# Optimization experiments

Hardware: AMD Instinct MI355X
Metric: run time of the kernel (lower is better)

## Reference

```python
import jax, jax.numpy as jnp
import numpy as np

# Static config matching init_kwargs / input_specs
B, CIN, H, W = 4, 64, 128, 128
COUT, K, DG = 64, 3, 8
STRIDE, PAD, DIL = 1, 1, 1
HO = (H + 2 * PAD - DIL * (K - 1) - 1) // STRIDE + 1
WO = (W + 2 * PAD - DIL * (K - 1) - 1) // STRIDE + 1
KK = K * K
CG = CIN // DG  # channels per deformable group


def setup_inputs() -> dict:
    key = jax.random.key(0)
    k1, k2, k3, k4 = jax.random.split(key, 4)
    x = jax.random.normal(k1, (B, CIN, H, W), jnp.float32)
    offset = jax.random.normal(k2, (B, 2 * DG * KK, HO, WO), jnp.float32)
    s = 1.0 / np.sqrt(CIN * KK)  # matches reset_parameters stdv / fan_in bound
    weight = jax.random.uniform(k3, (COUT, CIN, K, K), jnp.float32, -s, s)
    bias = jax.random.uniform(k4, (COUT,), jnp.float32, -s, s)
    return {"x": x, "offset": offset, "weight": weight, "bias": bias}


def _deform_conv(x, offset, weight, bias):
    # offset layout (DCNv1): [B, DG * KK * 2, Ho, Wo], per kernel point (dy, dx)
    off = offset.reshape(B, DG, KK, 2, HO, WO)
    khs = (jnp.repeat(jnp.arange(K), K) * DIL).astype(jnp.float32)  # [KK] kernel dy
    kws = (jnp.tile(jnp.arange(K), K) * DIL).astype(jnp.float32)    # [KK] kernel dx
    gy = (jnp.arange(HO) * STRIDE - PAD).astype(jnp.float32)        # [Ho] base y
    gx = (jnp.arange(WO) * STRIDE - PAD).astype(jnp.float32)        # [Wo] base x
    # sampling positions: [B, DG, KK, Ho, Wo]
    py = gy[None, None, None, :, None] + khs[None, None, :, None, None] + off[:, :, :, 0]
    px = gx[None, None, None, None, :] + kws[None, None, :, None, None] + off[:, :, :, 1]
    y0 = jnp.floor(py)
    x0 = jnp.floor(px)
    ly = py - y0  # fractional parts
    lx = px - x0
    xg = x.reshape(B, DG, CG, H * W)  # channels grouped by deformable group

    def corner(yc, xc, wgt):
        # zero-padded bilinear: out-of-bounds corners contribute 0
        valid = (yc >= 0) & (yc < H) & (xc >= 0) & (xc < W)
        idx = (jnp.clip(yc, 0, H - 1) * W + jnp.clip(xc, 0, W - 1)).astype(jnp.int32)
        v = jnp.take_along_axis(xg, idx.reshape(B, DG, 1, KK * HO * WO), axis=3)
        v = v.reshape(B, DG, CG, KK, HO, WO)
        w = jnp.where(valid, wgt, 0.0)  # [B, DG, KK, Ho, Wo]
        return v * w[:, :, None]

    cols = (corner(y0, x0, (1.0 - ly) * (1.0 - lx))
            + corner(y0, x0 + 1.0, (1.0 - ly) * lx)
            + corner(y0 + 1.0, x0, ly * (1.0 - lx))
            + corner(y0 + 1.0, x0 + 1.0, ly * lx))  # [B, DG, CG, KK, Ho, Wo]

    wk = weight.reshape(COUT, DG, CG, KK)  # groups == 1
    out = jnp.einsum('bgcpyx,ogcp->boyx', cols, wk)
    return out + bias[None, :, None, None]


def reference(x, offset, weight, bias):
    return _deform_conv(x, offset, weight, bias)
```

## Files before the change

kernel.cpp:

```cpp
#include <hip/hip_runtime.h>

#define BB    4
#define CINT  64
#define HH    128
#define WW    128
#define COUT  64
#define DGN   8
#define CG    8
#define KKN   9
#define HO    128
#define WO    128
#define HOWO  16384
#define HWSZ  (HH * WW)
#define NCHUNK 18

typedef __bf16 bf16x8 __attribute__((ext_vector_type(8)));
typedef float  f32x4  __attribute__((ext_vector_type(4)));

static __device__ __forceinline__ ushort f2bf(float f) {
    unsigned u = __builtin_bit_cast(unsigned, f);
    u += 0x7fffu + ((u >> 16) & 1u);
    return (ushort)(u >> 16);
}
static __device__ __forceinline__ float bf2f(ushort u) {
    return __builtin_bit_cast(float, (unsigned)u << 16);
}

__global__ void prep_w(const float* __restrict__ wgt, uint4* __restrict__ wout) {
    int i = blockIdx.x * 256 + threadIdx.x;
    if (i >= NCHUNK * 4 * 64) return;
    int lane = i & 63;
    int mt   = (i >> 6) & 3;
    int kt   = i >> 8;
    int m = lane & 15, quad = lane >> 4;
    int o = mt * 16 + m;
    union { ushort u[8]; uint4 v; } pk;
#pragma unroll
    for (int j = 0; j < 8; ++j) {
        int k   = kt * 32 + quad * 8 + j;
        int gkk = k >> 3, c = k & 7;
        int g   = gkk / 9, kk = gkk - 9 * g;
        pk.u[j] = f2bf(wgt[(o * CINT + g * CG + c) * KKN + kk]);
    }
    wout[i] = pk.v;
}

__global__ void prep_x(const float* __restrict__ x, uint4* __restrict__ xh) {
    int i  = blockIdx.x * 256 + threadIdx.x;
    int yx = i & (HWSZ - 1);
    int bg = i >> 14;
    const float* xp = x + (size_t)bg * CG * HWSZ + yx;
    union { ushort u[8]; uint4 v; } pk;
#pragma unroll
    for (int c = 0; c < CG; ++c) pk.u[c] = f2bf(xp[c * HWSZ]);
    xh[i] = pk.v;
}

__global__ __launch_bounds__(256, 6) void dcn_mfma(
    const uint4* __restrict__ xh, const float* __restrict__ off,
    const uint4* __restrict__ wq, const float* __restrict__ bias,
    float* __restrict__ out)
{
    __shared__ __align__(16) ushort col[2][64][40];
    __shared__ float sbias[COUT];

    const int tid  = threadIdx.x;
    const int wave = tid >> 6;
    const int lane = tid & 63;
    const int px   = tid & 63;
    const int p    = wave;

    const int pix_base = blockIdx.x * 64;
    const int b        = pix_base >> 14;
    const int rem_base = pix_base & 16383;
    const int rem      = rem_base + px;
    const int ho = rem >> 7, wo = rem & 127;
    const float fy0 = (float)(ho - 1);
    const float fx0 = (float)(wo - 1);

    if (tid < COUT) sbias[tid] = bias[tid];

    f32x4 acc[4];
#pragma unroll
    for (int mt = 0; mt < 4; ++mt) acc[mt] = (f32x4){0.f, 0.f, 0.f, 0.f};

    auto produce = [&](int ch) {
        int gkk = ch * 4 + p;
        int g = gkk / 9, kk = gkk - 9 * g;
        const float* offp = off + ((size_t)((b * DGN + g) * KKN + kk) * 2) * HOWO + rem;
        float dy = offp[0];
        float dx = offp[HOWO];
        float py  = fy0 + (float)(kk / 3) + dy;
        float pxx = fx0 + (float)(kk - (kk / 3) * 3) + dx;
        float y0f = floorf(py), x0f = floorf(pxx);
        int y0 = (int)y0f, x0 = (int)x0f;
        float ly = py - y0f, lx = pxx - x0f;
        float hy = 1.f - ly, hx = 1.f - lx;
        float w00 = hy * hx, w01 = hy * lx, w10 = ly * hx, w11 = ly * lx;
        int y1 = y0 + 1, x1 = x0 + 1;
        bool vy0 = (unsigned)y0 < (unsigned)HH, vy1 = (unsigned)y1 < (unsigned)HH;
        bool vx0 = (unsigned)x0 < (unsigned)WW, vx1 = (unsigned)x1 < (unsigned)WW;
        if (!(vy0 && vx0)) w00 = 0.f;
        if (!(vy0 && vx1)) w01 = 0.f;
        if (!(vy1 && vx0)) w10 = 0.f;
        if (!(vy1 && vx1)) w11 = 0.f;
        int y0c = min(max(y0, 0), HH - 1), y1c = min(max(y1, 0), HH - 1);
        int x0c = min(max(x0, 0), WW - 1), x1c = min(max(x1, 0), WW - 1);
        const uint4* xgp = xh + (size_t)(b * DGN + g) * HWSZ;
        uint4 q00 = xgp[y0c * WW + x0c];
        uint4 q01 = xgp[y0c * WW + x1c];
        uint4 q10 = xgp[y1c * WW + x0c];
        uint4 q11 = xgp[y1c * WW + x1c];
        const ushort* u00 = (const ushort*)&q00;
        const ushort* u01 = (const ushort*)&q01;
        const ushort* u10 = (const ushort*)&q10;
        const ushort* u11 = (const ushort*)&q11;
        union { ushort u[8]; uint4 v; } pk;
#pragma unroll
        for (int c = 0; c < CG; ++c) {
            float v = w00 * bf2f(u00[c]) + w01 * bf2f(u01[c])
                    + w10 * bf2f(u10[c]) + w11 * bf2f(u11[c]);
            pk.u[c] = f2bf(v);
        }
        *(uint4*)&col[ch & 1][px][p * 8] = pk.v;
    };

    produce(0);

    const int brow  = wave * 16 + (lane & 15);
    const int bkoff = (lane >> 4) * 8;

    for (int ch = 0; ch < NCHUNK; ++ch) {
        __syncthreads();
        bf16x8 bfrag = *(const bf16x8*)&col[ch & 1][brow][bkoff];
#pragma unroll
        for (int mt = 0; mt < 4; ++mt) {
            bf16x8 afrag = __builtin_bit_cast(bf16x8, wq[(ch * 4 + mt) * 64 + lane]);
            acc[mt] = __builtin_amdgcn_mfma_f32_16x16x32_bf16(afrag, bfrag, acc[mt], 0, 0, 0);
        }
        if (ch + 1 < NCHUNK) produce(ch + 1);
    }

    const int n = lane & 15, quad = lane >> 4;
    const int rem_out = rem_base + wave * 16 + n;
    float* outp = out + (size_t)b * COUT * HOWO + rem_out;
#pragma unroll
    for (int mt = 0; mt < 4; ++mt) {
#pragma unroll
        for (int r = 0; r < 4; ++r) {
            int o = mt * 16 + quad * 4 + r;
            outp[(size_t)o * HOWO] = acc[mt][r] + sbias[o];
        }
    }
}

extern "C" void kernel_launch(void* const* d_in, const int* in_sizes, int n_in,
                              void* d_out, int out_size, void* d_ws, size_t ws_size,
                              hipStream_t stream) {
    const float* x    = (const float*)d_in[0];
    const float* off  = (const float*)d_in[1];
    const float* wgt  = (const float*)d_in[2];
    const float* bias = (const float*)d_in[3];
    float* out = (float*)d_out;

    uint4* xh = (uint4*)d_ws;
    uint4* wq = (uint4*)((char*)d_ws + 8388608);

    prep_x<<<dim3(BB * DGN * HWSZ / 256), dim3(256), 0, stream>>>(x, xh);
    prep_w<<<dim3(NCHUNK), dim3(256), 0, stream>>>(wgt, wq);
    dcn_mfma<<<dim3(BB * HO * WO / 64), dim3(256), 0, stream>>>(xh, off, wq, bias, out);
}
```

Before: 120.8 us.

## Shrink pixel tile to 32, split output channels across waves, swizzle block order

The fused deformable-conv kernel now handles 32 pixels per block instead of 64. Each block processes 8 gkk slots per chunk across 9 chunks rather than 4 slots across 18, which halves the number of barriers. Waves split the output-channel tiles (two M-tiles each) and the pixel halves, and block IDs are swizzled so consecutive blocks spread across distant tiles. Together with a higher occupancy bound, this aims for more parallelism and fewer sync points. The cost is that each weight fragment is reused across fewer pixels, and the extra blocks and swizzle may hurt L2 locality of offset and input reads.

```diff
diff --git a/kernel.cpp b/kernel.cpp
--- a/kernel.cpp
+++ b/kernel.cpp
@@ -12,7 +12,9 @@
 #define WO    128
 #define HOWO  16384
 #define HWSZ  (HH * WW)
-#define NCHUNK 18
+#define NKT   18
+#define NCH   9
+#define CROW  72
 
 typedef __bf16 bf16x8 __attribute__((ext_vector_type(8)));
 typedef float  f32x4  __attribute__((ext_vector_type(4)));
@@ -28,7 +30,7 @@
 
 __global__ void prep_w(const float* __restrict__ wgt, uint4* __restrict__ wout) {
     int i = blockIdx.x * 256 + threadIdx.x;
-    if (i >= NCHUNK * 4 * 64) return;
+    if (i >= NKT * 4 * 64) return;
     int lane = i & 63;
     int mt   = (i >> 6) & 3;
     int kt   = i >> 8;
@@ -56,36 +58,39 @@
     xh[i] = pk.v;
 }
 
-__global__ __launch_bounds__(256, 6) void dcn_mfma(
+__global__ __launch_bounds__(256, 8) void dcn_mfma(
     const uint4* __restrict__ xh, const float* __restrict__ off,
     const uint4* __restrict__ wq, const float* __restrict__ bias,
     float* __restrict__ out)
 {
-    __shared__ __align__(16) ushort col[2][64][40];
+    __shared__ __align__(16) ushort col[2][32][CROW];
     __shared__ float sbias[COUT];
 
     const int tid  = threadIdx.x;
     const int wave = tid >> 6;
     const int lane = tid & 63;
-    const int px   = tid & 63;
-    const int p    = wave;
 
-    const int pix_base = blockIdx.x * 64;
+    const int bid  = blockIdx.x;
+    const int tile = ((bid & 7) << 8) | (bid >> 3);
+    const int pix_base = tile * 32;
     const int b        = pix_base >> 14;
     const int rem_base = pix_base & 16383;
-    const int rem      = rem_base + px;
+
+    const int ppx = tid & 31;
+    const int q   = tid >> 5;
+    const int rem = rem_base + ppx;
     const int ho = rem >> 7, wo = rem & 127;
     const float fy0 = (float)(ho - 1);
     const float fx0 = (float)(wo - 1);
 
     if (tid < COUT) sbias[tid] = bias[tid];
 
-    f32x4 acc[4];
-#pragma unroll
-    for (int mt = 0; mt < 4; ++mt) acc[mt] = (f32x4){0.f, 0.f, 0.f, 0.f};
+    f32x4 acc[2];
+    acc[0] = (f32x4){0.f, 0.f, 0.f, 0.f};
+    acc[1] = (f32x4){0.f, 0.f, 0.f, 0.f};
 
     auto produce = [&](int ch) {
-        int gkk = ch * 4 + p;
+        int gkk = ch * 8 + q;
         int g = gkk / 9, kk = gkk - 9 * g;
         const float* offp = off + ((size_t)((b * DGN + g) * KKN + kk) * 2) * HOWO + rem;
         float dy = offp[0];
@@ -122,34 +127,39 @@
                     + w10 * bf2f(u10[c]) + w11 * bf2f(u11[c]);
             pk.u[c] = f2bf(v);
         }
-        *(uint4*)&col[ch & 1][px][p * 8] = pk.v;
+        *(uint4*)&col[ch & 1][ppx][q * 8] = pk.v;
     };
 
     produce(0);
 
-    const int brow  = wave * 16 + (lane & 15);
-    const int bkoff = (lane >> 4) * 8;
+    const int n = lane & 15, quad = lane >> 4;
+    const int nh = wave & 1, mp = wave >> 1;
+    const int brow = nh * 16 + n;
 
-    for (int ch = 0; ch < NCHUNK; ++ch) {
+    for (int ch = 0; ch < NCH; ++ch) {
         __syncthreads();
-        bf16x8 bfrag = *(const bf16x8*)&col[ch & 1][brow][bkoff];
+        bf16x8 bf0 = *(const bf16x8*)&col[ch & 1][brow][quad * 8];
+        bf16x8 bf1 = *(const bf16x8*)&col[ch & 1][brow][32 + quad * 8];
+        const int kt0 = ch * 2;
 #pragma unroll
-        for (int mt = 0; mt < 4; ++mt) {
-            bf16x8 afrag = __builtin_bit_cast(bf16x8, wq[(ch * 4 + mt) * 64 + lane]);
-            acc[mt] = __builtin_amdgcn_mfma_f32_16x16x32_bf16(afrag, bfrag, acc[mt], 0, 0, 0);
+        for (int ti = 0; ti < 2; ++ti) {
+            const int mt = mp * 2 + ti;
+            bf16x8 a0 = __builtin_bit_cast(bf16x8, wq[(kt0 * 4 + mt) * 64 + lane]);
+            bf16x8 a1 = __builtin_bit_cast(bf16x8, wq[((kt0 + 1) * 4 + mt) * 64 + lane]);
+            acc[ti] = __builtin_amdgcn_mfma_f32_16x16x32_bf16(a0, bf0, acc[ti], 0, 0, 0);
+            acc[ti] = __builtin_amdgcn_mfma_f32_16x16x32_bf16(a1, bf1, acc[ti], 0, 0, 0);
         }
-        if (ch + 1 < NCHUNK) produce(ch + 1);
+        if (ch + 1 < NCH) produce(ch + 1);
     }
 
-    const int n = lane & 15, quad = lane >> 4;
-    const int rem_out = rem_base + wave * 16 + n;
+    const int rem_out = rem_base + nh * 16 + n;
     float* outp = out + (size_t)b * COUT * HOWO + rem_out;
 #pragma unroll
-    for (int mt = 0; mt < 4; ++mt) {
+    for (int ti = 0; ti < 2; ++ti) {
 #pragma unroll
         for (int r = 0; r < 4; ++r) {
-            int o = mt * 16 + quad * 4 + r;
-            outp[(size_t)o * HOWO] = acc[mt][r] + sbias[o];
+            int o = (mp * 2 + ti) * 16 + quad * 4 + r;
+            outp[(size_t)o * HOWO] = acc[ti][r] + sbias[o];
         }
     }
 }
@@ -167,6 +177,6 @@
     uint4* wq = (uint4*)((char*)d_ws + 8388608);
 
     prep_x<<<dim3(BB * DGN * HWSZ / 256), dim3(256), 0, stream>>>(x, xh);
-    prep_w<<<dim3(NCHUNK), dim3(256), 0, stream>>>(wgt, wq);
-    dcn_mfma<<<dim3(BB * HO * WO / 64), dim3(256), 0, stream>>>(xh, off, wq, bias, out);
+    prep_w<<<dim3(NKT), dim3(256), 0, stream>>>(wgt, wq);
+    dcn_mfma<<<dim3(BB * HO * WO / 32), dim3(256), 0, stream>>>(xh, off, wq, bias, out);
 }
```

Result: no change. 121.7 us (+0.7%).

## Build MFMA B fragments in registers, dropping LDS staging and barriers

Applied to the files above, without the earlier changes.

Each wave now samples the bilinear columns for its own 16 pixels in the exact lane layout the MFMA B operand needs, so the shared-memory double buffer and per-chunk __syncthreads are gone. The K loop is fully unrolled with weight fragments loaded per step, bias is read directly from global memory, and block indices are swizzled so consecutive blocks cover spread-out pixel tiles. The cost is more registers (launch bounds lowered to 4 blocks per CU) and a different gather access pattern for each lane.

```diff
diff --git a/kernel.cpp b/kernel.cpp
--- a/kernel.cpp
+++ b/kernel.cpp
@@ -12,7 +12,7 @@
 #define WO    128
 #define HOWO  16384
 #define HWSZ  (HH * WW)
-#define NCHUNK 18
+#define NKT   18
 
 typedef __bf16 bf16x8 __attribute__((ext_vector_type(8)));
 typedef float  f32x4  __attribute__((ext_vector_type(4)));
@@ -28,7 +28,7 @@
 
 __global__ void prep_w(const float* __restrict__ wgt, uint4* __restrict__ wout) {
     int i = blockIdx.x * 256 + threadIdx.x;
-    if (i >= NCHUNK * 4 * 64) return;
+    if (i >= NKT * 4 * 64) return;
     int lane = i & 63;
     int mt   = (i >> 6) & 3;
     int kt   = i >> 8;
@@ -56,36 +56,41 @@
     xh[i] = pk.v;
 }
 
-__global__ __launch_bounds__(256, 6) void dcn_mfma(
+__global__ __launch_bounds__(256, 4) void dcn_mfma(
     const uint4* __restrict__ xh, const float* __restrict__ off,
     const uint4* __restrict__ wq, const float* __restrict__ bias,
     float* __restrict__ out)
 {
-    __shared__ __align__(16) ushort col[2][64][40];
-    __shared__ float sbias[COUT];
-
     const int tid  = threadIdx.x;
     const int wave = tid >> 6;
     const int lane = tid & 63;
-    const int px   = tid & 63;
-    const int p    = wave;
+    const int n    = lane & 15;
+    const int quad = lane >> 4;
 
-    const int pix_base = blockIdx.x * 64;
+    const int bid  = blockIdx.x;
+    const int tile = ((bid & 7) << 7) | (bid >> 3);
+    const int pix_base = tile * 64 + wave * 16;
     const int b        = pix_base >> 14;
     const int rem_base = pix_base & 16383;
-    const int rem      = rem_base + px;
+    const int rem      = rem_base + n;
     const int ho = rem >> 7, wo = rem & 127;
     const float fy0 = (float)(ho - 1);
     const float fx0 = (float)(wo - 1);
-
-    if (tid < COUT) sbias[tid] = bias[tid];
 
     f32x4 acc[4];
 #pragma unroll
     for (int mt = 0; mt < 4; ++mt) acc[mt] = (f32x4){0.f, 0.f, 0.f, 0.f};
 
-    auto produce = [&](int ch) {
-        int gkk = ch * 4 + p;
+    const uint4* xb = xh + (size_t)b * DGN * HWSZ;
+
+#pragma unroll
+    for (int kt = 0; kt < NKT; ++kt) {
+        uint4 aw0 = wq[(kt * 4 + 0) * 64 + lane];
+        uint4 aw1 = wq[(kt * 4 + 1) * 64 + lane];
+        uint4 aw2 = wq[(kt * 4 + 2) * 64 + lane];
+        uint4 aw3 = wq[(kt * 4 + 3) * 64 + lane];
+
+        int gkk = kt * 4 + quad;
         int g = gkk / 9, kk = gkk - 9 * g;
         const float* offp = off + ((size_t)((b * DGN + g) * KKN + kk) * 2) * HOWO + rem;
         float dy = offp[0];
@@ -106,7 +111,7 @@
         if (!(vy1 && vx1)) w11 = 0.f;
         int y0c = min(max(y0, 0), HH - 1), y1c = min(max(y1, 0), HH - 1);
         int x0c = min(max(x0, 0), WW - 1), x1c = min(max(x1, 0), WW - 1);
-        const uint4* xgp = xh + (size_t)(b * DGN + g) * HWSZ;
+        const uint4* xgp = xb + (size_t)g * HWSZ;
         uint4 q00 = xgp[y0c * WW + x0c];
         uint4 q01 = xgp[y0c * WW + x1c];
         uint4 q10 = xgp[y1c * WW + x0c];
@@ -115,41 +120,33 @@
         const ushort* u01 = (const ushort*)&q01;
         const ushort* u10 = (const ushort*)&q10;
         const ushort* u11 = (const ushort*)&q11;
-        union { ushort u[8]; uint4 v; } pk;
+        union { ushort u[8]; bf16x8 v; } pk;
 #pragma unroll
         for (int c = 0; c < CG; ++c) {
             float v = w00 * bf2f(u00[c]) + w01 * bf2f(u01[c])
                     + w10 * bf2f(u10[c]) + w11 * bf2f(u11[c]);
             pk.u[c] = f2bf(v);
         }
-        *(uint4*)&col[ch & 1][px][p * 8] = pk.v;
-    };
+        bf16x8 bfrag = pk.v;
 
-    produce(0);
-
-    const int brow  = wave * 16 + (lane & 15);
-    const int bkoff = (lane >> 4) * 8;
-
-    for (int ch = 0; ch < NCHUNK; ++ch) {
-        __syncthreads();
-        bf16x8 bfrag = *(const bf16x8*)&col[ch & 1][brow][bkoff];
-#pragma unroll
-        for (int mt = 0; mt < 4; ++mt) {
-            bf16x8 afrag = __builtin_bit_cast(bf16x8, wq[(ch * 4 + mt) * 64 + lane]);
-            acc[mt] = __builtin_amdgcn_mfma_f32_16x16x32_bf16(afrag, bfrag, acc[mt], 0, 0, 0);
-        }
-        if (ch + 1 < NCHUNK) produce(ch + 1);
+        acc[0] = __builtin_amdgcn_mfma_f32_16x16x32_bf16(
+                     __builtin_bit_cast(bf16x8, aw0), bfrag, acc[0], 0, 0, 0);
+        acc[1] = __builtin_amdgcn_mfma_f32_16x16x32_bf16(
+                     __builtin_bit_cast(bf16x8, aw1), bfrag, acc[1], 0, 0, 0);
+        acc[2] = __builtin_amdgcn_mfma_f32_16x16x32_bf16(
+                     __builtin_bit_cast(bf16x8, aw2), bfrag, acc[2], 0, 0, 0);
+        acc[3] = __builtin_amdgcn_mfma_f32_16x16x32_bf16(
+                     __builtin_bit_cast(bf16x8, aw3), bfrag, acc[3], 0, 0, 0);
     }
 
-    const int n = lane & 15, quad = lane >> 4;
-    const int rem_out = rem_base + wave * 16 + n;
-    float* outp = out + (size_t)b * COUT * HOWO + rem_out;
+    float* outp = out + (size_t)b * COUT * HOWO + rem_base + n;
 #pragma unroll
     for (int mt = 0; mt < 4; ++mt) {
+        const float4 bq = *(const float4*)&bias[mt * 16 + quad * 4];
 #pragma unroll
         for (int r = 0; r < 4; ++r) {
             int o = mt * 16 + quad * 4 + r;
-            outp[(size_t)o * HOWO] = acc[mt][r] + sbias[o];
+            outp[(size_t)o * HOWO] = acc[mt][r] + ((const float*)&bq)[r];
         }
     }
 }
@@ -167,6 +164,6 @@
     uint4* wq = (uint4*)((char*)d_ws + 8388608);
 
     prep_x<<<dim3(BB * DGN * HWSZ / 256), dim3(256), 0, stream>>>(x, xh);
-    prep_w<<<dim3(NCHUNK), dim3(256), 0, stream>>>(wgt, wq);
+    prep_w<<<dim3(NKT), dim3(256), 0, stream>>>(wgt, wq);
     dcn_mfma<<<dim3(BB * HO * WO / 64), dim3(256), 0, stream>>>(xh, off, wq, bias, out);
 }
```

Measured after the change: 123.0 us. About the same (+1.8%).
